# Kernel optimization log

Measured on AMD Instinct MI355X. Metric: run time of the kernel, lower is better.

## Reference

```python
import jax, jax.numpy as jnp
import numpy as np

B, OBS, E, H, NT, A, NH = 65536, 128, 64, 128, 7, 16, 4
HD = E // NH  # head dim = 16


def setup_inputs() -> dict:
    key = jax.random.key(0)
    ks = jax.random.split(key, 16)
    def p(i, shape, s=0.05):
        return jax.random.normal(ks[i], shape, jnp.float32) * s
    return {
        "obs": jax.random.normal(ks[0], (B, OBS), jnp.float32),
        "prev_belief": jax.random.normal(ks[1], (B, H), jnp.float32),
        "teammate_hidden": jax.random.normal(ks[2], (B, NT, H), jnp.float32),
        # obs_encoder: Linear(OBS->E), ReLU, Linear(E->E), ReLU
        "W1": p(3, (E, OBS)), "b1": jnp.zeros((E,), jnp.float32),
        "W2": p(4, (E, E)), "b2": jnp.zeros((E,), jnp.float32),
        # hidden_proj: Linear(H->E)
        "Wp": p(5, (E, H)), "bp": jnp.zeros((E,), jnp.float32),
        # nn.MultiheadAttention packed in-proj + out-proj
        "in_proj_w": p(6, (3 * E, E)), "in_proj_b": jnp.zeros((3 * E,), jnp.float32),
        "out_proj_w": p(7, (E, E)), "out_proj_b": jnp.zeros((E,), jnp.float32),
        # GRUCell(input=2E, hidden=H): gate order r, z, n (torch convention)
        "gru_wih": p(8, (3 * H, 2 * E)), "gru_whh": p(9, (3 * H, H)),
        "gru_bih": jnp.zeros((3 * H,), jnp.float32), "gru_bhh": jnp.zeros((3 * H,), jnp.float32),
        # policy head (gain 0.01 init -> small scale)
        "Wpol": p(10, (A, H), 0.01), "bpol": jnp.zeros((A,), jnp.float32),
    }


def reference(obs, prev_belief, teammate_hidden,
              W1, b1, W2, b2, Wp, bp,
              in_proj_w, in_proj_b, out_proj_w, out_proj_b,
              gru_wih, gru_whh, gru_bih, gru_bhh, Wpol, bpol):
    # 1. observation encoder (2-layer ReLU MLP)
    h_obs = jax.nn.relu(jax.nn.relu(obs @ W1.T + b1) @ W2.T + b2)          # [B,E]
    # 2-3. project own belief (query) and teammate hiddens (keys/values)
    q_in = prev_belief @ Wp.T + bp                                          # [B,E]
    kv_in = teammate_hidden @ Wp.T + bp                                     # [B,NT,E]
    # 4. multi-head attention (query len 1 over NT teammates), torch MHA semantics
    Wq, Wk, Wv = jnp.split(in_proj_w, 3, axis=0)
    bq, bk, bv = jnp.split(in_proj_b, 3, axis=0)
    q = (q_in @ Wq.T + bq).reshape(B, NH, HD)                               # [B,NH,HD]
    k = (kv_in @ Wk.T + bk).reshape(B, NT, NH, HD)                          # [B,NT,NH,HD]
    v = (kv_in @ Wv.T + bv).reshape(B, NT, NH, HD)
    scores = jnp.einsum('bhd,bthd->bht', q, k) / np.float32(np.sqrt(HD))    # [B,NH,NT]
    attn = jax.nn.softmax(scores, axis=-1)
    ctx = jnp.einsum('bht,bthd->bhd', attn, v).reshape(B, E)                # concat heads
    context = ctx @ out_proj_w.T + out_proj_b                               # [B,E]
    attn_weights = attn.mean(axis=1)                                        # avg over heads -> [B,NT]
    # 5. GRUCell update on [h_obs || context]
    x = jnp.concatenate([h_obs, context], axis=-1)                          # [B,2E]
    gi = x @ gru_wih.T + gru_bih
    gh = prev_belief @ gru_whh.T + gru_bhh
    ir, iz, inn = jnp.split(gi, 3, axis=-1)
    hr, hz, hn = jnp.split(gh, 3, axis=-1)
    r = jax.nn.sigmoid(ir + hr)
    z = jax.nn.sigmoid(iz + hz)
    n = jnp.tanh(inn + r * hn)
    belief = (1.0 - z) * n + z * prev_belief                                # [B,H]
    # 6. policy head
    action_logits = belief @ Wpol.T + bpol                                  # [B,A]
    return action_logits, belief, attn_weights
```

## Files before the change

kernel.cpp:

```cpp
#include <hip/hip_runtime.h>

#define DEVINL __device__ __forceinline__

typedef unsigned short u16;
typedef unsigned long long u64;
typedef __attribute__((ext_vector_type(8))) short bf16x8;
typedef __attribute__((ext_vector_type(16))) float f32x16;

#define NB   65536
#define OBSD 128
#define ED   64
#define HD_  128
#define NT   7
#define NA   16

#define OFF_W1   0
#define OFF_W2   8192
#define OFF_WP   12288
#define OFF_INP  20480
#define OFF_OUTP 32768
#define OFF_WIH  36864
#define OFF_WHH  86016
#define OFF_POL  135168
#define W_TOTAL  137216

DEVINL u16 f2bf(float f) {
  unsigned u = __float_as_uint(f);
  u += 0x7fff + ((u >> 16) & 1);
  return (u16)(u >> 16);
}
DEVINL float bf2f(u16 h) { return __uint_as_float(((unsigned)h) << 16); }

DEVINL f32x16 mfma(bf16x8 a, bf16x8 b, f32x16 c) {
  return __builtin_amdgcn_mfma_f32_32x32x16_bf16(a, b, c, 0, 0, 0);
}
DEVINL f32x16 zero16() {
  f32x16 z;
#pragma unroll
  for (int i = 0; i < 16; ++i) z[i] = 0.f;
  return z;
}

DEVINL bf16x8 ldsA(const u16* p) {
  union { bf16x8 v; u64 u[2]; } t;
  t.u[0] = *(const u64*)p;
  t.u[1] = *(const u64*)(p + 4);
  return t.v;
}

template<int KS>
DEVINL f32x16 gemm_acc(const u16* __restrict__ bufA, int S, int aRow, int khalf,
                       const u16* __restrict__ wRow, f32x16 acc) {
  const u16* ap = bufA + aRow * S + khalf;
  const u16* bp = wRow + khalf;
#pragma unroll
  for (int ks = 0; ks < KS; ++ks) {
    bf16x8 a = ldsA(ap + ks * 16);
    bf16x8 b = *(const bf16x8*)(bp + ks * 16);
    acc = mfma(a, b, acc);
  }
  return acc;
}

DEVINL void epiLDS(const f32x16& acc, float bias, int rowOff, int col,
                   u16* buf, int S, bool relu) {
#pragma unroll
  for (int r = 0; r < 16; ++r) {
    int row = rowOff + (r & 3) + 8 * (r >> 2);
    float v = acc[r] + bias;
    if (relu) v = fmaxf(v, 0.f);
    buf[row * S + col] = f2bf(v);
  }
}

DEVINL float sigf(float x) { return 1.f / (1.f + __expf(-x)); }

__global__ void pack_weights(const float* __restrict__ W1, const float* __restrict__ W2,
                             const float* __restrict__ Wp, const float* __restrict__ inpw,
                             const float* __restrict__ outpw, const float* __restrict__ wih,
                             const float* __restrict__ whh, const float* __restrict__ wpol,
                             u16* __restrict__ ws) {
  int i = blockIdx.x * 256 + threadIdx.x;
  const float* src; int off;
  if      (i < OFF_W2)  { src = W1;    off = OFF_W1; }
  else if (i < OFF_WP)  { src = W2;    off = OFF_W2; }
  else if (i < OFF_INP) { src = Wp;    off = OFF_WP; }
  else if (i < OFF_OUTP){ src = inpw;  off = OFF_INP; }
  else if (i < OFF_WIH) { src = outpw; off = OFF_OUTP; }
  else if (i < OFF_WHH) { src = wih;   off = OFF_WIH; }
  else if (i < OFF_POL) { src = whh;   off = OFF_WHH; }
  else if (i < W_TOTAL) { src = wpol;  off = OFF_POL; }
  else return;
  ws[i] = f2bf(src[i - off]);
}

__global__ __launch_bounds__(256, 2)
void aerial_main(const float* __restrict__ obs, const float* __restrict__ pb,
                 const float* __restrict__ th,
                 const float* __restrict__ b1, const float* __restrict__ b2,
                 const float* __restrict__ bp,
                 const float* __restrict__ inpb, const float* __restrict__ outpb,
                 const float* __restrict__ bih, const float* __restrict__ bhh,
                 const float* __restrict__ bpol,
                 const u16* __restrict__ wsb,
                 float* __restrict__ outLog, float* __restrict__ outBel,
                 float* __restrict__ outAttn) {
  __shared__ u16 bufP[64 * 132];
  __shared__ u16 bufB[64 * 132];
  __shared__ u16 bufH1[64 * 68];
  __shared__ u16 bufHO[64 * 68];
  __shared__ u16 bufQ[64 * 68];

  const int tid   = threadIdx.x;
  const int lane  = tid & 63;
  const int m     = lane & 31;
  const int half  = lane >> 5;
  const int khalf = half * 8;
  const int wv    = tid >> 6;
  const int mt    = wv & 1;
  const int nh    = wv >> 1;
  const int aRow  = 32 * mt + m;
  const int rowOff = 32 * mt + 4 * half;
  const int col64 = nh * 32 + m;
  const int gRow0 = blockIdx.x * 64;

  const u16* wsW1   = wsb + OFF_W1;
  const u16* wsW2   = wsb + OFF_W2;
  const u16* wsWP   = wsb + OFF_WP;
  const u16* wsINP  = wsb + OFF_INP;
  const u16* wsOUTP = wsb + OFF_OUTP;
  const u16* wsWIH  = wsb + OFF_WIH;
  const u16* wsWHH  = wsb + OFF_WHH;
  const u16* wsPOL  = wsb + OFF_POL;

  auto stage = [&](const float* src, int srcStride, u16* dst) {
#pragma unroll
    for (int i = 0; i < 8; ++i) {
      int f4 = tid + i * 256;
      int row = f4 >> 5;
      int c4  = f4 & 31;
      float4 v = *(const float4*)(src + (size_t)row * srcStride + c4 * 4);
      ushort4 o;
      o.x = f2bf(v.x); o.y = f2bf(v.y); o.z = f2bf(v.z); o.w = f2bf(v.w);
      *(ushort4*)(dst + row * 132 + c4 * 4) = o;
    }
  };

  stage(obs + (size_t)gRow0 * OBSD, OBSD, bufB);
  stage(pb  + (size_t)gRow0 * HD_,  HD_,  bufP);
  __syncthreads();

  {
    f32x16 acc = gemm_acc<8>(bufB, 132, aRow, khalf, wsW1 + col64 * 128, zero16());
    epiLDS(acc, b1[col64], rowOff, col64, bufH1, 68, true);
  }
  {
    f32x16 acc = gemm_acc<8>(bufP, 132, aRow, khalf, wsWP + col64 * 128, zero16());
    epiLDS(acc, bp[col64], rowOff, col64, bufQ, 68, false);
  }
  __syncthreads();

  {
    f32x16 acc = gemm_acc<4>(bufH1, 68, aRow, khalf, wsW2 + col64 * 64, zero16());
    epiLDS(acc, b2[col64], rowOff, col64, bufHO, 68, true);
  }
  {
    f32x16 acc = gemm_acc<4>(bufQ, 68, aRow, khalf, wsINP + col64 * 64, zero16());
    epiLDS(acc, inpb[col64], rowOff, col64, bufB, 132, false);
  }
  __syncthreads();

  const int b  = tid >> 2;
  const int hh = tid & 3;
  float qreg[16];
#pragma unroll
  for (int d = 0; d < 16; ++d) qreg[d] = bf2f(bufB[b * 132 + hh * 16 + d]);
  float ctx[16];
#pragma unroll
  for (int d = 0; d < 16; ++d) ctx[d] = 0.f;
  float l = 0.f, parr[NT];
  __syncthreads();

  for (int t = 0; t < NT; ++t) {
    stage(th + (size_t)gRow0 * (NT * HD_) + t * HD_, NT * HD_, bufB);
    __syncthreads();
    {
      f32x16 acc = gemm_acc<8>(bufB, 132, aRow, khalf, wsWP + col64 * 128, zero16());
      epiLDS(acc, bp[col64], rowOff, col64, bufH1, 68, false);
    }
    __syncthreads();
    {
      f32x16 acc = gemm_acc<4>(bufH1, 68, aRow, khalf, wsINP + (64 + col64) * 64, zero16());
      epiLDS(acc, inpb[64 + col64], rowOff, col64, bufQ, 68, false);
    }
    __syncthreads();
    {
      float s = 0.f;
#pragma unroll
      for (int d = 0; d < 16; ++d) s += qreg[d] * bf2f(bufQ[b * 68 + hh * 16 + d]);
      float p = __expf(s * 0.25f);
      l += p; parr[t] = p;
    }
    __syncthreads();
    {
      f32x16 acc = gemm_acc<4>(bufH1, 68, aRow, khalf, wsINP + (128 + col64) * 64, zero16());
      epiLDS(acc, inpb[128 + col64], rowOff, col64, bufQ, 68, false);
    }
    __syncthreads();
    {
      float p = parr[t];
#pragma unroll
      for (int d = 0; d < 16; ++d) ctx[d] += p * bf2f(bufQ[b * 68 + hh * 16 + d]);
    }
  }

  {
    float linv = 1.f / l;
#pragma unroll
    for (int t = 0; t < NT; ++t) {
      float a = parr[t] * linv;
      a += __shfl_xor(a, 1);
      a += __shfl_xor(a, 2);
      if (hh == 0) outAttn[(size_t)(gRow0 + b) * NT + t] = a * 0.25f;
    }
#pragma unroll
    for (int d = 0; d < 16; ++d) bufH1[b * 68 + hh * 16 + d] = f2bf(ctx[d] * linv);
  }
  __syncthreads();

  {
    f32x16 acc = gemm_acc<4>(bufH1, 68, aRow, khalf, wsOUTP + col64 * 64, zero16());
    epiLDS(acc, outpb[col64], rowOff, col64, bufQ, 68, false);
  }
  __syncthreads();

  bf16x8 ax[8], apb[8];
#pragma unroll
  for (int ks = 0; ks < 4; ++ks) ax[ks]     = ldsA(bufHO + aRow * 68 + ks * 16 + khalf);
#pragma unroll
  for (int ks = 0; ks < 4; ++ks) ax[4 + ks] = ldsA(bufQ  + aRow * 68 + ks * 16 + khalf);
#pragma unroll
  for (int ks = 0; ks < 8; ++ks) apb[ks]    = ldsA(bufP  + aRow * 132 + ks * 16 + khalf);

#pragma unroll
  for (int hj = 0; hj < 2; ++hj) {
    int jt = nh * 32 + hj * 64;
    int j  = jt + m;
    const u16* wr = wsWIH + (0 * HD_ + j) * 128;
    const u16* wz = wsWIH + (1 * HD_ + j) * 128;
    const u16* wn = wsWIH + (2 * HD_ + j) * 128;
    const u16* vr = wsWHH + (0 * HD_ + j) * 128;
    const u16* vz = wsWHH + (1 * HD_ + j) * 128;
    const u16* vn = wsWHH + (2 * HD_ + j) * 128;
    f32x16 ar = zero16(), az = zero16(), ai = zero16(), ah = zero16();
#pragma unroll
    for (int ks = 0; ks < 8; ++ks) {
      int ko = ks * 16 + khalf;
      ar = mfma(ax[ks], *(const bf16x8*)(wr + ko), ar);
      az = mfma(ax[ks], *(const bf16x8*)(wz + ko), az);
      ai = mfma(ax[ks], *(const bf16x8*)(wn + ko), ai);
    }
#pragma unroll
    for (int ks = 0; ks < 8; ++ks) {
      int ko = ks * 16 + khalf;
      ar = mfma(apb[ks], *(const bf16x8*)(vr + ko), ar);
      az = mfma(apb[ks], *(const bf16x8*)(vz + ko), az);
      ah = mfma(apb[ks], *(const bf16x8*)(vn + ko), ah);
    }
    float br_ = bih[j] + bhh[j];
    float bz_ = bih[HD_ + j] + bhh[HD_ + j];
    float bi_ = bih[2 * HD_ + j];
    float bh_ = bhh[2 * HD_ + j];
#pragma unroll
    for (int r = 0; r < 16; ++r) {
      int row = rowOff + (r & 3) + 8 * (r >> 2);
      float rr = sigf(ar[r] + br_);
      float zz = sigf(az[r] + bz_);
      float xn = ai[r] + bi_ + rr * (ah[r] + bh_);
      xn = fminf(fmaxf(xn, -15.f), 15.f);
      float tt = __expf(2.f * xn);
      float nn = (tt - 1.f) / (tt + 1.f);
      float pv = bf2f(bufP[row * 132 + j]);
      float bel = (1.f - zz) * nn + zz * pv;
      outBel[(size_t)(gRow0 + row) * HD_ + j] = bel;
      bufB[row * 132 + j] = f2bf(bel);
    }
  }
  __syncthreads();

  if (nh == 0) {
    int nclamp = (m < 16) ? m : 15;
    f32x16 acc = gemm_acc<8>(bufB, 132, aRow, khalf, wsPOL + nclamp * 128, zero16());
    if (m < 16) {
      float bv = bpol[m];
#pragma unroll
      for (int r = 0; r < 16; ++r) {
        int row = rowOff + (r & 3) + 8 * (r >> 2);
        outLog[(size_t)(gRow0 + row) * NA + m] = acc[r] + bv;
      }
    }
  }
}

extern "C" void kernel_launch(void* const* d_in, const int* in_sizes, int n_in,
                              void* d_out, int out_size, void* d_ws, size_t ws_size,
                              hipStream_t stream) {
  const float* obs   = (const float*)d_in[0];
  const float* pb    = (const float*)d_in[1];
  const float* th    = (const float*)d_in[2];
  const float* W1    = (const float*)d_in[3];
  const float* b1    = (const float*)d_in[4];
  const float* W2    = (const float*)d_in[5];
  const float* b2    = (const float*)d_in[6];
  const float* Wp    = (const float*)d_in[7];
  const float* bp    = (const float*)d_in[8];
  const float* inpw  = (const float*)d_in[9];
  const float* inpb  = (const float*)d_in[10];
  const float* outpw = (const float*)d_in[11];
  const float* outpb = (const float*)d_in[12];
  const float* wih   = (const float*)d_in[13];
  const float* whh   = (const float*)d_in[14];
  const float* bih   = (const float*)d_in[15];
  const float* bhh   = (const float*)d_in[16];
  const float* wpol  = (const float*)d_in[17];
  const float* bpol  = (const float*)d_in[18];

  u16* wsb = (u16*)d_ws;
  float* outLog  = (float*)d_out;
  float* outBel  = outLog + (size_t)NB * NA;
  float* outAttn = outBel + (size_t)NB * HD_;

  pack_weights<<<W_TOTAL / 256, 256, 0, stream>>>(W1, W2, Wp, inpw, outpw, wih, whh,
                                                  wpol, wsb);
  aerial_main<<<NB / 64, 256, 0, stream>>>(obs, pb, th, b1, b2, bp, inpb, outpb,
                                           bih, bhh, bpol, wsb, outLog, outBel, outAttn);
}
```

Before: 454.9 us.

## Fold projection weights into attention and GRU weights, prefetch teammate tiles

Result: slower. 615.0 us (+35.2%).

```diff
diff --git a/kernel.cpp b/kernel.cpp
--- a/kernel.cpp
+++ b/kernel.cpp
@@ -16,13 +16,14 @@
 
 #define OFF_W1   0
 #define OFF_W2   8192
-#define OFF_WP   12288
-#define OFF_INP  20480
-#define OFF_OUTP 32768
+#define OFF_WQP  12288
+#define OFF_WKP  20480
+#define OFF_WVP  28672
 #define OFF_WIH  36864
 #define OFF_WHH  86016
 #define OFF_POL  135168
 #define W_TOTAL  137216
+#define NBIAS    576
 
 DEVINL u16 f2bf(float f) {
   unsigned u = __float_as_uint(f);
@@ -48,6 +49,17 @@
   return t.v;
 }
 
+DEVINL bf16x8 gfrag(const float* p) {
+  float4 a = ((const float4*)p)[0];
+  float4 b = ((const float4*)p)[1];
+  bf16x8 r;
+  r[0] = (short)f2bf(a.x); r[1] = (short)f2bf(a.y);
+  r[2] = (short)f2bf(a.z); r[3] = (short)f2bf(a.w);
+  r[4] = (short)f2bf(b.x); r[5] = (short)f2bf(b.y);
+  r[6] = (short)f2bf(b.z); r[7] = (short)f2bf(b.w);
+  return r;
+}
+
 template<int KS>
 DEVINL f32x16 gemm_acc(const u16* __restrict__ bufA, int S, int aRow, int khalf,
                        const u16* __restrict__ wRow, f32x16 acc) {
@@ -73,43 +85,84 @@
   }
 }
 
+DEVINL void rd16(const u16* p, float* o) {
+  union { u64 u[4]; u16 s[16]; } t;
+  t.u[0] = ((const u64*)p)[0]; t.u[1] = ((const u64*)p)[1];
+  t.u[2] = ((const u64*)p)[2]; t.u[3] = ((const u64*)p)[3];
+#pragma unroll
+  for (int d = 0; d < 16; ++d) o[d] = bf2f(t.s[d]);
+}
+
 DEVINL float sigf(float x) { return 1.f / (1.f + __expf(-x)); }
 
-__global__ void pack_weights(const float* __restrict__ W1, const float* __restrict__ W2,
-                             const float* __restrict__ Wp, const float* __restrict__ inpw,
-                             const float* __restrict__ outpw, const float* __restrict__ wih,
+__global__ void prep_weights(const float* __restrict__ W1, const float* __restrict__ W2,
+                             const float* __restrict__ Wp, const float* __restrict__ bp,
+                             const float* __restrict__ inpw, const float* __restrict__ inpb,
+                             const float* __restrict__ outpw, const float* __restrict__ outpb,
+                             const float* __restrict__ wih, const float* __restrict__ bih,
                              const float* __restrict__ whh, const float* __restrict__ wpol,
                              u16* __restrict__ ws) {
   int i = blockIdx.x * 256 + threadIdx.x;
-  const float* src; int off;
-  if      (i < OFF_W2)  { src = W1;    off = OFF_W1; }
-  else if (i < OFF_WP)  { src = W2;    off = OFF_W2; }
-  else if (i < OFF_INP) { src = Wp;    off = OFF_WP; }
-  else if (i < OFF_OUTP){ src = inpw;  off = OFF_INP; }
-  else if (i < OFF_WIH) { src = outpw; off = OFF_OUTP; }
-  else if (i < OFF_WHH) { src = wih;   off = OFF_WIH; }
-  else if (i < OFF_POL) { src = whh;   off = OFF_WHH; }
-  else if (i < W_TOTAL) { src = wpol;  off = OFF_POL; }
-  else return;
-  ws[i] = f2bf(src[i - off]);
-}
-
-__global__ __launch_bounds__(256, 2)
+  if (i < W_TOTAL) {
+    float v;
+    if (i < OFF_W2)       v = W1[i];
+    else if (i < OFF_WQP) v = W2[i - OFF_W2];
+    else if (i < OFF_WIH) {
+      int o = i - OFF_WQP;
+      int mat = o >> 13;
+      int e = (o >> 7) & 63;
+      int h = o & 127;
+      const float* wr = inpw + (mat * 64 + e) * 64;
+      float acc = 0.f;
+#pragma unroll 4
+      for (int c = 0; c < 64; ++c) acc += wr[c] * Wp[c * 128 + h];
+      v = (mat == 0) ? acc * 0.25f : acc;
+    } else if (i < OFF_WHH) {
+      int o = i - OFF_WIH;
+      int g = o >> 7, c = o & 127;
+      if (c < 64) v = wih[g * 128 + c];
+      else {
+        int d = c - 64;
+        float acc = 0.f;
+#pragma unroll 4
+        for (int c2 = 0; c2 < 64; ++c2) acc += wih[g * 128 + 64 + c2] * outpw[c2 * 64 + d];
+        v = acc;
+      }
+    }
+    else if (i < OFF_POL) v = whh[i - OFF_WHH];
+    else                  v = wpol[i - OFF_POL];
+    ws[i] = f2bf(v);
+  } else if (i < W_TOTAL + NBIAS) {
+    float* wsF = (float*)(ws + W_TOTAL);
+    int o = i - W_TOTAL;
+    float acc = 0.f;
+    if (o < 192) {
+      int mat = o >> 6, e = o & 63;
+      const float* wr = inpw + (mat * 64 + e) * 64;
+      for (int c = 0; c < 64; ++c) acc += wr[c] * bp[c];
+      acc += inpb[mat * 64 + e];
+      if (mat == 0) acc *= 0.25f;
+    } else {
+      int g = o - 192;
+      for (int c = 0; c < 64; ++c) acc += wih[g * 128 + 64 + c] * outpb[c];
+      acc += bih[g];
+    }
+    wsF[o] = acc;
+  }
+}
+
+__global__ __launch_bounds__(256, 3)
 void aerial_main(const float* __restrict__ obs, const float* __restrict__ pb,
                  const float* __restrict__ th,
                  const float* __restrict__ b1, const float* __restrict__ b2,
-                 const float* __restrict__ bp,
-                 const float* __restrict__ inpb, const float* __restrict__ outpb,
-                 const float* __restrict__ bih, const float* __restrict__ bhh,
-                 const float* __restrict__ bpol,
+                 const float* __restrict__ bpol, const float* __restrict__ bhh,
                  const u16* __restrict__ wsb,
                  float* __restrict__ outLog, float* __restrict__ outBel,
                  float* __restrict__ outAttn) {
-  __shared__ u16 bufP[64 * 132];
-  __shared__ u16 bufB[64 * 132];
-  __shared__ u16 bufH1[64 * 68];
+  __shared__ u16 bufT[64 * 132];
+  __shared__ u16 bufK[64 * 68];
+  __shared__ u16 bufV[64 * 68];
   __shared__ u16 bufHO[64 * 68];
-  __shared__ u16 bufQ[64 * 68];
 
   const int tid   = threadIdx.x;
   const int lane  = tid & 63;
@@ -124,94 +177,101 @@
   const int col64 = nh * 32 + m;
   const int gRow0 = blockIdx.x * 64;
 
-  const u16* wsW1   = wsb + OFF_W1;
-  const u16* wsW2   = wsb + OFF_W2;
-  const u16* wsWP   = wsb + OFF_WP;
-  const u16* wsINP  = wsb + OFF_INP;
-  const u16* wsOUTP = wsb + OFF_OUTP;
-  const u16* wsWIH  = wsb + OFF_WIH;
-  const u16* wsWHH  = wsb + OFF_WHH;
-  const u16* wsPOL  = wsb + OFF_POL;
-
-  auto stage = [&](const float* src, int srcStride, u16* dst) {
+  const float* wsF = (const float*)(wsb + W_TOTAL);
+
+  float4 sreg[8];
+  auto issue = [&](int t) {
 #pragma unroll
     for (int i = 0; i < 8; ++i) {
       int f4 = tid + i * 256;
-      int row = f4 >> 5;
-      int c4  = f4 & 31;
-      float4 v = *(const float4*)(src + (size_t)row * srcStride + c4 * 4);
+      int row = f4 >> 5, c4 = f4 & 31;
+      sreg[i] = *(const float4*)(th + ((size_t)(gRow0 + row) * NT + t) * HD_ + c4 * 4);
+    }
+  };
+  auto swrite = [&]() {
+#pragma unroll
+    for (int i = 0; i < 8; ++i) {
+      int f4 = tid + i * 256;
+      int row = f4 >> 5, c4 = f4 & 31;
       ushort4 o;
-      o.x = f2bf(v.x); o.y = f2bf(v.y); o.z = f2bf(v.z); o.w = f2bf(v.w);
-      *(ushort4*)(dst + row * 132 + c4 * 4) = o;
+      o.x = f2bf(sreg[i].x); o.y = f2bf(sreg[i].y);
+      o.z = f2bf(sreg[i].z); o.w = f2bf(sreg[i].w);
+      *(ushort4*)(bufT + row * 132 + c4 * 4) = o;
     }
   };
 
-  stage(obs + (size_t)gRow0 * OBSD, OBSD, bufB);
-  stage(pb  + (size_t)gRow0 * HD_,  HD_,  bufP);
+  issue(0);
+  {
+    const float* arow = pb + (size_t)(gRow0 + aRow) * HD_ + khalf;
+    const u16* brow = wsb + OFF_WQP + col64 * 128 + khalf;
+    f32x16 acc = zero16();
+#pragma unroll
+    for (int ks = 0; ks < 8; ++ks)
+      acc = mfma(gfrag(arow + ks * 16), *(const bf16x8*)(brow + ks * 16), acc);
+    epiLDS(acc, wsF[col64], rowOff, col64, bufV, 68, false);
+  }
+  {
+    const float* arow = obs + (size_t)(gRow0 + aRow) * OBSD + khalf;
+    const u16* brow = wsb + OFF_W1 + col64 * 128 + khalf;
+    f32x16 acc = zero16();
+#pragma unroll
+    for (int ks = 0; ks < 8; ++ks)
+      acc = mfma(gfrag(arow + ks * 16), *(const bf16x8*)(brow + ks * 16), acc);
+    epiLDS(acc, b1[col64], rowOff, col64, bufK, 68, true);
+  }
+  swrite();
   __syncthreads();
 
   {
-    f32x16 acc = gemm_acc<8>(bufB, 132, aRow, khalf, wsW1 + col64 * 128, zero16());
-    epiLDS(acc, b1[col64], rowOff, col64, bufH1, 68, true);
-  }
-  {
-    f32x16 acc = gemm_acc<8>(bufP, 132, aRow, khalf, wsWP + col64 * 128, zero16());
-    epiLDS(acc, bp[col64], rowOff, col64, bufQ, 68, false);
-  }
-  __syncthreads();
-
-  {
-    f32x16 acc = gemm_acc<4>(bufH1, 68, aRow, khalf, wsW2 + col64 * 64, zero16());
+    f32x16 acc = gemm_acc<4>(bufK, 68, aRow, khalf, wsb + OFF_W2 + col64 * 64, zero16());
     epiLDS(acc, b2[col64], rowOff, col64, bufHO, 68, true);
   }
-  {
-    f32x16 acc = gemm_acc<4>(bufQ, 68, aRow, khalf, wsINP + col64 * 64, zero16());
-    epiLDS(acc, inpb[col64], rowOff, col64, bufB, 132, false);
-  }
-  __syncthreads();
-
   const int b  = tid >> 2;
   const int hh = tid & 3;
   float qreg[16];
-#pragma unroll
-  for (int d = 0; d < 16; ++d) qreg[d] = bf2f(bufB[b * 132 + hh * 16 + d]);
+  rd16(bufV + b * 68 + hh * 16, qreg);
+  issue(1);
+  __syncthreads();
+
+  const float bkF = wsF[64 + col64];
+  const float bvF = wsF[128 + col64];
   float ctx[16];
 #pragma unroll
   for (int d = 0; d < 16; ++d) ctx[d] = 0.f;
   float l = 0.f, parr[NT];
-  __syncthreads();
-
+
+#pragma unroll
   for (int t = 0; t < NT; ++t) {
-    stage(th + (size_t)gRow0 * (NT * HD_) + t * HD_, NT * HD_, bufB);
+    bf16x8 af[8];
+#pragma unroll
+    for (int ks = 0; ks < 8; ++ks) af[ks] = ldsA(bufT + aRow * 132 + ks * 16 + khalf);
+    const u16* bKp = wsb + OFF_WKP + col64 * 128 + khalf;
+    const u16* bVp = wsb + OFF_WVP + col64 * 128 + khalf;
+    f32x16 aK = zero16(), aV = zero16();
+#pragma unroll
+    for (int ks = 0; ks < 8; ++ks) {
+      aK = mfma(af[ks], *(const bf16x8*)(bKp + ks * 16), aK);
+      aV = mfma(af[ks], *(const bf16x8*)(bVp + ks * 16), aV);
+    }
+    epiLDS(aK, bkF, rowOff, col64, bufK, 68, false);
+    epiLDS(aV, bvF, rowOff, col64, bufV, 68, false);
     __syncthreads();
+
     {
-      f32x16 acc = gemm_acc<8>(bufB, 132, aRow, khalf, wsWP + col64 * 128, zero16());
-      epiLDS(acc, bp[col64], rowOff, col64, bufH1, 68, false);
-    }
+      float kv[16];
+      rd16(bufK + b * 68 + hh * 16, kv);
+      float s = 0.f;
+#pragma unroll
+      for (int d = 0; d < 16; ++d) s += qreg[d] * kv[d];
+      float p = __expf(s);
+      l += p; parr[t] = p;
+      rd16(bufV + b * 68 + hh * 16, kv);
+#pragma unroll
+      for (int d = 0; d < 16; ++d) ctx[d] += p * kv[d];
+    }
+    if (t < NT - 1) swrite();
+    if (t < NT - 2) issue(t + 2);
     __syncthreads();
-    {
-      f32x16 acc = gemm_acc<4>(bufH1, 68, aRow, khalf, wsINP + (64 + col64) * 64, zero16());
-      epiLDS(acc, inpb[64 + col64], rowOff, col64, bufQ, 68, false);
-    }
-    __syncthreads();
-    {
-      float s = 0.f;
-#pragma unroll
-      for (int d = 0; d < 16; ++d) s += qreg[d] * bf2f(bufQ[b * 68 + hh * 16 + d]);
-      float p = __expf(s * 0.25f);
-      l += p; parr[t] = p;
-    }
-    __syncthreads();
-    {
-      f32x16 acc = gemm_acc<4>(bufH1, 68, aRow, khalf, wsINP + (128 + col64) * 64, zero16());
-      epiLDS(acc, inpb[128 + col64], rowOff, col64, bufQ, 68, false);
-    }
-    __syncthreads();
-    {
-      float p = parr[t];
-#pragma unroll
-      for (int d = 0; d < 16; ++d) ctx[d] += p * bf2f(bufQ[b * 68 + hh * 16 + d]);
-    }
   }
 
   {
@@ -224,34 +284,28 @@
       if (hh == 0) outAttn[(size_t)(gRow0 + b) * NT + t] = a * 0.25f;
     }
 #pragma unroll
-    for (int d = 0; d < 16; ++d) bufH1[b * 68 + hh * 16 + d] = f2bf(ctx[d] * linv);
+    for (int d = 0; d < 16; ++d) bufV[b * 68 + hh * 16 + d] = f2bf(ctx[d] * linv);
   }
   __syncthreads();
 
-  {
-    f32x16 acc = gemm_acc<4>(bufH1, 68, aRow, khalf, wsOUTP + col64 * 64, zero16());
-    epiLDS(acc, outpb[col64], rowOff, col64, bufQ, 68, false);
-  }
-  __syncthreads();
-
   bf16x8 ax[8], apb[8];
 #pragma unroll
   for (int ks = 0; ks < 4; ++ks) ax[ks]     = ldsA(bufHO + aRow * 68 + ks * 16 + khalf);
 #pragma unroll
-  for (int ks = 0; ks < 4; ++ks) ax[4 + ks] = ldsA(bufQ  + aRow * 68 + ks * 16 + khalf);
-#pragma unroll
-  for (int ks = 0; ks < 8; ++ks) apb[ks]    = ldsA(bufP  + aRow * 132 + ks * 16 + khalf);
+  for (int ks = 0; ks < 4; ++ks) ax[4 + ks] = ldsA(bufV  + aRow * 68 + ks * 16 + khalf);
+  const float* pbrow = pb + (size_t)(gRow0 + aRow) * HD_ + khalf;
+#pragma unroll
+  for (int ks = 0; ks < 8; ++ks) apb[ks] = gfrag(pbrow + ks * 16);
 
 #pragma unroll
   for (int hj = 0; hj < 2; ++hj) {
-    int jt = nh * 32 + hj * 64;
-    int j  = jt + m;
-    const u16* wr = wsWIH + (0 * HD_ + j) * 128;
-    const u16* wz = wsWIH + (1 * HD_ + j) * 128;
-    const u16* wn = wsWIH + (2 * HD_ + j) * 128;
-    const u16* vr = wsWHH + (0 * HD_ + j) * 128;
-    const u16* vz = wsWHH + (1 * HD_ + j) * 128;
-    const u16* vn = wsWHH + (2 * HD_ + j) * 128;
+    int j = nh * 32 + hj * 64 + m;
+    const u16* wr = wsb + OFF_WIH + (size_t)(0 * HD_ + j) * 128;
+    const u16* wz = wsb + OFF_WIH + (size_t)(1 * HD_ + j) * 128;
+    const u16* wn = wsb + OFF_WIH + (size_t)(2 * HD_ + j) * 128;
+    const u16* vr = wsb + OFF_WHH + (size_t)(0 * HD_ + j) * 128;
+    const u16* vz = wsb + OFF_WHH + (size_t)(1 * HD_ + j) * 128;
+    const u16* vn = wsb + OFF_WHH + (size_t)(2 * HD_ + j) * 128;
     f32x16 ar = zero16(), az = zero16(), ai = zero16(), ah = zero16();
 #pragma unroll
     for (int ks = 0; ks < 8; ++ks) {
@@ -267,10 +321,10 @@
       az = mfma(apb[ks], *(const bf16x8*)(vz + ko), az);
       ah = mfma(apb[ks], *(const bf16x8*)(vn + ko), ah);
     }
-    float br_ = bih[j] + bhh[j];
-    float bz_ = bih[HD_ + j] + bhh[HD_ + j];
-    float bi_ = bih[2 * HD_ + j];
-    float bh_ = bhh[2 * HD_ + j];
+    float br_ = wsF[192 + j] + bhh[j];
+    float bz_ = wsF[192 + 128 + j] + bhh[128 + j];
+    float bi_ = wsF[192 + 256 + j];
+    float bh_ = bhh[256 + j];
 #pragma unroll
     for (int r = 0; r < 16; ++r) {
       int row = rowOff + (r & 3) + 8 * (r >> 2);
@@ -280,17 +334,17 @@
       xn = fminf(fmaxf(xn, -15.f), 15.f);
       float tt = __expf(2.f * xn);
       float nn = (tt - 1.f) / (tt + 1.f);
-      float pv = bf2f(bufP[row * 132 + j]);
+      float pv = pb[(size_t)(gRow0 + row) * HD_ + j];
       float bel = (1.f - zz) * nn + zz * pv;
       outBel[(size_t)(gRow0 + row) * HD_ + j] = bel;
-      bufB[row * 132 + j] = f2bf(bel);
+      bufT[row * 132 + j] = f2bf(bel);
     }
   }
   __syncthreads();
 
   if (nh == 0) {
     int nclamp = (m < 16) ? m : 15;
-    f32x16 acc = gemm_acc<8>(bufB, 132, aRow, khalf, wsPOL + nclamp * 128, zero16());
+    f32x16 acc = gemm_acc<8>(bufT, 132, aRow, khalf, wsb + OFF_POL + nclamp * 128, zero16());
     if (m < 16) {
       float bv = bpol[m];
 #pragma unroll
@@ -330,8 +384,8 @@
   float* outBel  = outLog + (size_t)NB * NA;
   float* outAttn = outBel + (size_t)NB * HD_;
 
-  pack_weights<<<W_TOTAL / 256, 256, 0, stream>>>(W1, W2, Wp, inpw, outpw, wih, whh,
-                                                  wpol, wsb);
-  aerial_main<<<NB / 64, 256, 0, stream>>>(obs, pb, th, b1, b2, bp, inpb, outpb,
-                                           bih, bhh, bpol, wsb, outLog, outBel, outAttn);
-}
+  prep_weights<<<(W_TOTAL + NBIAS + 255) / 256, 256, 0, stream>>>(
+      W1, W2, Wp, bp, inpw, inpb, outpw, outpb, wih, bih, whh, wpol, wsb);
+  aerial_main<<<NB / 64, 256, 0, stream>>>(obs, pb, th, b1, b2, bpol, bhh, wsb,
+                                           outLog, outBel, outAttn);
+}
```
